# Performance work log

Measured on AMD Instinct MI355X. Metric: run time of the kernel, lower is better.

## Reference

```python
import jax, jax.numpy as jnp
import numpy as np

N_EMBED = 768
NUM_HEADS = 12
HEAD_DIM = N_EMBED // NUM_HEADS
B, L = 4, 2048


def setup_inputs() -> dict:
    key = jax.random.key(0)
    ks = jax.random.split(key, 11)
    s = 0.02
    return {
        "key": jax.random.normal(ks[0], (B, L, N_EMBED), jnp.float32),
        "query": jax.random.normal(ks[1], (B, L, N_EMBED), jnp.float32),
        "value": jax.random.normal(ks[2], (B, L, N_EMBED), jnp.float32),
        "Wk": jax.random.normal(ks[3], (N_EMBED, N_EMBED), jnp.float32) * s,
        "bk": jnp.zeros((N_EMBED,), jnp.float32),
        "Wq": jax.random.normal(ks[4], (N_EMBED, N_EMBED), jnp.float32) * s,
        "bq": jnp.zeros((N_EMBED,), jnp.float32),
        "Wv": jax.random.normal(ks[5], (N_EMBED, N_EMBED), jnp.float32) * s,
        "bv": jnp.zeros((N_EMBED,), jnp.float32),
        "Wfc": jax.random.normal(ks[6], (N_EMBED, N_EMBED), jnp.float32) * s,
        "bfc": jnp.zeros((N_EMBED,), jnp.float32),
    }


def reference(key, query, value, Wk, bk, Wq, bq, Wv, bv, Wfc, bfc):
    # Linear projections (torch Linear: x @ W.T + b)
    k = key @ Wk.T + bk      # [B, Lk, D]
    q = query @ Wq.T + bq    # [B, Lq, D]
    v = value @ Wv.T + bv    # [B, Lv, D]
    Bsz, Lq = q.shape[0], q.shape[1]
    k = k.reshape(Bsz, -1, NUM_HEADS, HEAD_DIM)
    q = q.reshape(Bsz, Lq, NUM_HEADS, HEAD_DIM)
    v = v.reshape(Bsz, -1, NUM_HEADS, HEAD_DIM)
    # Full [B, H, Lq, Lk] score tensor, scaled by sqrt(n_embed) (faithful to source)
    energies = jnp.einsum("nqhd,nkhd->nhqk", q, k)
    attn = jax.nn.softmax(energies / jnp.sqrt(jnp.float32(N_EMBED)), axis=3)
    out = jnp.einsum("nhql,nlhd->nqhd", attn, v).reshape(Bsz, Lq, N_EMBED)
    return out @ Wfc.T + bfc
```

## Files before the change

### kernel.cpp

```cpp
#include <hip/hip_runtime.h>
#include <hip/hip_bf16.h>
#include <math.h>

#define NEMB 768
#define NH   12
#define HD   64
#define BSZ  4
#define SEQ  2048
#define MTOT (BSZ * SEQ)

#define SCALE_LOG2E 0.0520587833f

typedef short bf16x8 __attribute__((ext_vector_type(8)));
typedef short short4v __attribute__((ext_vector_type(4)));
typedef float f32x4 __attribute__((ext_vector_type(4)));
typedef unsigned u32x4 __attribute__((ext_vector_type(4)));

__device__ __forceinline__ short f2bf(float f) {
  __bf16 h = (__bf16)f;
  return __builtin_bit_cast(short, h);
}

__device__ __forceinline__ void g2l16(const short* g, short* l) {
  __builtin_amdgcn_global_load_lds((const __attribute__((address_space(1))) unsigned*)g,
                                   (__attribute__((address_space(3))) unsigned*)l, 16, 0, 0);
}

__device__ __forceinline__ int swz(int x) { return (x ^ (x >> 3)) & 7; }

__global__ __launch_bounds__(256) void cvt_all(
    const float* __restrict__ i0, const float* __restrict__ i1, const float* __restrict__ i2,
    const float* __restrict__ i3, const float* __restrict__ i4, const float* __restrict__ i5,
    const float* __restrict__ i6,
    short* __restrict__ o0, short* __restrict__ o1, short* __restrict__ o2,
    short* __restrict__ o3, short* __restrict__ o4, short* __restrict__ o5,
    short* __restrict__ o6) {
  const int ACT4 = (MTOT * NEMB) / 4;
  const int WGT4 = (NEMB * NEMB) / 4;
  const float* in; short* out; int n4;
  switch (blockIdx.y) {
    case 0: in = i0; out = o0; n4 = ACT4; break;
    case 1: in = i1; out = o1; n4 = ACT4; break;
    case 2: in = i2; out = o2; n4 = ACT4; break;
    case 3: in = i3; out = o3; n4 = WGT4; break;
    case 4: in = i4; out = o4; n4 = WGT4; break;
    case 5: in = i5; out = o5; n4 = WGT4; break;
    default: in = i6; out = o6; n4 = WGT4; break;
  }
  int i = blockIdx.x * 256 + threadIdx.x;
  if (i >= n4) return;
  float4 f = reinterpret_cast<const float4*>(in)[i];
  short4v s; s[0] = f2bf(f.x); s[1] = f2bf(f.y); s[2] = f2bf(f.z); s[3] = f2bf(f.w);
  reinterpret_cast<short4v*>(out)[i] = s;
}

__global__ __launch_bounds__(256) void gemm_qkv(
    const short* __restrict__ A0, const short* __restrict__ A1, const short* __restrict__ A2,
    const short* __restrict__ W0, const short* __restrict__ W1, const short* __restrict__ W2,
    const float* __restrict__ b0, const float* __restrict__ b1, const float* __restrict__ b2,
    short* __restrict__ O0, short* __restrict__ O1, short* __restrict__ O2) {
  __shared__ __align__(16) short As[128 * 32];
  __shared__ __align__(16) short Bs[128 * 32];
  const short* A; const short* W; const float* bias; short* O; float scl;
  switch (blockIdx.z) {
    case 0:  A = A0; W = W0; bias = b0; O = O0; scl = SCALE_LOG2E; break;
    case 1:  A = A1; W = W1; bias = b1; O = O1; scl = 1.f; break;
    default: A = A2; W = W2; bias = b2; O = O2; scl = 1.f; break;
  }
  const int tid = threadIdx.x;
  const int lane = tid & 63, w = tid >> 6;
  const int wr = w >> 1, wc = w & 1;
  const int l15 = lane & 15, l4 = lane >> 4;
  const int m0 = blockIdx.x * 128, n0 = blockIdx.y * 128;

  f32x4 acc[4][4] = {};

  for (int k0 = 0; k0 < NEMB; k0 += 32) {
    __syncthreads();
#pragma unroll
    for (int i = 0; i < 2; ++i) {
      const int idx = tid + i * 256;
      const int row = idx >> 2, u = idx & 3;
      g2l16(A + (size_t)(m0 + row) * NEMB + k0 + u * 8, &As[idx * 8]);
      g2l16(W + (size_t)(n0 + row) * NEMB + k0 + u * 8, &Bs[idx * 8]);
    }
    __syncthreads();

    bf16x8 af[4], bfr[4];
#pragma unroll
    for (int m = 0; m < 4; ++m)
      af[m] = *reinterpret_cast<const bf16x8*>(&As[(wr * 64 + m * 16 + l15) * 32 + l4 * 8]);
#pragma unroll
    for (int n = 0; n < 4; ++n)
      bfr[n] = *reinterpret_cast<const bf16x8*>(&Bs[(wc * 64 + n * 16 + l15) * 32 + l4 * 8]);
#pragma unroll
    for (int m = 0; m < 4; ++m)
#pragma unroll
      for (int n = 0; n < 4; ++n)
        acc[m][n] = __builtin_amdgcn_mfma_f32_16x16x32_bf16(af[m], bfr[n], acc[m][n], 0, 0, 0);
  }

  float bj[4];
#pragma unroll
  for (int n = 0; n < 4; ++n) bj[n] = bias[n0 + wc * 64 + n * 16 + l15];
#pragma unroll
  for (int m = 0; m < 4; ++m)
#pragma unroll
    for (int n = 0; n < 4; ++n) {
      const int col = n0 + wc * 64 + n * 16 + l15;
#pragma unroll
      for (int r = 0; r < 4; ++r) {
        const int row = m0 + wr * 64 + m * 16 + l4 * 4 + r;
        O[(size_t)row * NEMB + col] = f2bf((acc[m][n][r] + bj[n]) * scl);
      }
    }
}

__global__ __launch_bounds__(256) void gemm_fc(
    const short* __restrict__ A, const short* __restrict__ W,
    const float* __restrict__ bias, float* __restrict__ C) {
  __shared__ __align__(16) short As[128 * 32];
  __shared__ __align__(16) short Bs[128 * 32];
  const int tid = threadIdx.x;
  const int lane = tid & 63, w = tid >> 6;
  const int wr = w >> 1, wc = w & 1;
  const int l15 = lane & 15, l4 = lane >> 4;
  const int m0 = blockIdx.x * 128, n0 = blockIdx.y * 128;

  f32x4 acc[4][4] = {};

  for (int k0 = 0; k0 < NEMB; k0 += 32) {
    __syncthreads();
#pragma unroll
    for (int i = 0; i < 2; ++i) {
      const int idx = tid + i * 256;
      const int row = idx >> 2, u = idx & 3;
      g2l16(A + (size_t)(m0 + row) * NEMB + k0 + u * 8, &As[idx * 8]);
      g2l16(W + (size_t)(n0 + row) * NEMB + k0 + u * 8, &Bs[idx * 8]);
    }
    __syncthreads();

    bf16x8 af[4], bfr[4];
#pragma unroll
    for (int m = 0; m < 4; ++m)
      af[m] = *reinterpret_cast<const bf16x8*>(&As[(wr * 64 + m * 16 + l15) * 32 + l4 * 8]);
#pragma unroll
    for (int n = 0; n < 4; ++n)
      bfr[n] = *reinterpret_cast<const bf16x8*>(&Bs[(wc * 64 + n * 16 + l15) * 32 + l4 * 8]);
#pragma unroll
    for (int m = 0; m < 4; ++m)
#pragma unroll
      for (int n = 0; n < 4; ++n)
        acc[m][n] = __builtin_amdgcn_mfma_f32_16x16x32_bf16(af[m], bfr[n], acc[m][n], 0, 0, 0);
  }

  float bj[4];
#pragma unroll
  for (int n = 0; n < 4; ++n) bj[n] = bias[n0 + wc * 64 + n * 16 + l15];
#pragma unroll
  for (int m = 0; m < 4; ++m)
#pragma unroll
    for (int n = 0; n < 4; ++n) {
      const int col = n0 + wc * 64 + n * 16 + l15;
#pragma unroll
      for (int r = 0; r < 4; ++r) {
        const int row = m0 + wr * 64 + m * 16 + l4 * 4 + r;
        C[(size_t)row * NEMB + col] = acc[m][n][r] + bj[n];
      }
    }
}

__global__ __launch_bounds__(256) void attn_mfma(const short* __restrict__ qp, const short* __restrict__ kp,
                                                 const short* __restrict__ vp, short* __restrict__ ao) {
  __shared__ __align__(16) short Ks[64 * 64];
  __shared__ __align__(16) short Vt[64 * 64];
  __shared__ __align__(16) short Ps[4][16 * 72];
  const int tid = threadIdx.x, lane = tid & 63, w = tid >> 6;
  const int l15 = lane & 15, l4 = lane >> 4;
  const int wg = blockIdx.x;
  const int nid = (wg & 7) * 192 + (wg >> 3);
  const int q0 = (nid & 31) * 64;
  const int bh = nid >> 5;
  const int b = bh / NH, h = bh - b * NH;
  const size_t abase = (size_t)b * SEQ * NEMB + h * HD;

  bf16x8 qf[2];
#pragma unroll
  for (int kb = 0; kb < 2; ++kb)
    qf[kb] = *reinterpret_cast<const bf16x8*>(
        &qp[abase + (size_t)(q0 + w * 16 + l15) * NEMB + kb * 32 + l4 * 8]);

  f32x4 o[4] = {};
  float lacc[4] = {0.f, 0.f, 0.f, 0.f};
  const int vd8 = tid & 7, vkv2 = tid >> 3;
  const int vu = vkv2 >> 2, vsub = vkv2 & 3;
  const int pch = l15 >> 3, pcl = l15 & 7;

  for (int kt = 0; kt < SEQ / 64; ++kt) {
    const short* vr = vp + abase + (size_t)(kt * 64 + vkv2 * 2) * NEMB + vd8 * 8;
    bf16x8 v0 = *reinterpret_cast<const bf16x8*>(vr);
    bf16x8 v1 = *reinterpret_cast<const bf16x8*>(vr + NEMB);
    __syncthreads();

#pragma unroll
    for (int i = 0; i < 2; ++i) {
      const int idx = tid + i * 256;
      const int row = idx >> 3, u = idx & 7;
      g2l16(kp + abase + (size_t)(kt * 64 + row) * NEMB + (u ^ swz(row)) * 8, &Ks[idx * 8]);
    }
    {
      u32x4 a0 = __builtin_bit_cast(u32x4, v0);
      u32x4 a1 = __builtin_bit_cast(u32x4, v1);
#pragma unroll
      for (int jj = 0; jj < 4; ++jj) {
        unsigned lo = __builtin_amdgcn_perm(a1[jj], a0[jj], 0x05040100u);
        unsigned hi = __builtin_amdgcn_perm(a1[jj], a0[jj], 0x07060302u);
        const int d0 = vd8 * 8 + jj * 2;
        *reinterpret_cast<unsigned*>(reinterpret_cast<char*>(Vt) + d0 * 128 + (vu ^ swz(d0)) * 16 + vsub * 4) = lo;
        *reinterpret_cast<unsigned*>(reinterpret_cast<char*>(Vt) + (d0 + 1) * 128 + (vu ^ swz(d0 + 1)) * 16 + vsub * 4) = hi;
      }
    }
    __syncthreads();

    f32x4 sf[4];
#pragma unroll
    for (int nf = 0; nf < 4; ++nf) {
      f32x4 a = {0.f, 0.f, 0.f, 0.f};
#pragma unroll
      for (int kb = 0; kb < 2; ++kb) {
        const int row = nf * 16 + l15;
        const int u = kb * 4 + l4;
        bf16x8 kf = *reinterpret_cast<const bf16x8*>(
            reinterpret_cast<char*>(Ks) + row * 128 + (u ^ swz(row)) * 16);
        a = __builtin_amdgcn_mfma_f32_16x16x32_bf16(qf[kb], kf, a, 0, 0, 0);
      }
      sf[nf] = a;
    }

#pragma unroll
    for (int nf = 0; nf < 4; ++nf)
#pragma unroll
      for (int r = 0; r < 4; ++r) {
        const float p = exp2f(sf[nf][r]);
        lacc[r] += p;
        Ps[w][(l4 * 4 + r) * 72 + (((nf * 2 + pch) ^ l4) << 3) + pcl] = f2bf(p);
      }

#pragma unroll
    for (int kb = 0; kb < 2; ++kb) {
      bf16x8 pf = *reinterpret_cast<const bf16x8*>(
          &Ps[w][l15 * 72 + (((kb * 4 + l4) ^ ((l15 >> 2) & 3)) << 3)]);
#pragma unroll
      for (int df = 0; df < 4; ++df) {
        const int d = df * 16 + l15;
        const int u = kb * 4 + l4;
        bf16x8 vf = *reinterpret_cast<const bf16x8*>(
            reinterpret_cast<char*>(Vt) + d * 128 + (u ^ swz(d)) * 16);
        o[df] = __builtin_amdgcn_mfma_f32_16x16x32_bf16(pf, vf, o[df], 0, 0, 0);
      }
    }
  }

#pragma unroll
  for (int r = 0; r < 4; ++r)
#pragma unroll
    for (int off = 1; off < 16; off <<= 1)
      lacc[r] += __shfl_xor(lacc[r], off, 64);

  float inv[4];
#pragma unroll
  for (int r = 0; r < 4; ++r) inv[r] = 1.f / lacc[r];

#pragma unroll
  for (int df = 0; df < 4; ++df)
#pragma unroll
    for (int r = 0; r < 4; ++r) {
      const int row = q0 + w * 16 + l4 * 4 + r;
      ao[abase + (size_t)row * NEMB + df * 16 + l15] = f2bf(o[df][r] * inv[r]);
    }
}

extern "C" void kernel_launch(void* const* d_in, const int* in_sizes, int n_in,
                              void* d_out, int out_size, void* d_ws, size_t ws_size,
                              hipStream_t stream) {
  const float* key   = (const float*)d_in[0];
  const float* query = (const float*)d_in[1];
  const float* value = (const float*)d_in[2];
  const float* Wk    = (const float*)d_in[3];
  const float* bk    = (const float*)d_in[4];
  const float* Wq    = (const float*)d_in[5];
  const float* bq    = (const float*)d_in[6];
  const float* Wv    = (const float*)d_in[7];
  const float* bv    = (const float*)d_in[8];
  const float* Wfc   = (const float*)d_in[9];
  const float* bfc   = (const float*)d_in[10];

  const size_t P = (size_t)MTOT * NEMB;
  const size_t WSZ = (size_t)NEMB * NEMB;
  short* ws  = (short*)d_ws;
  short* qb  = ws;
  short* kb2 = qb + P;
  short* vb2 = kb2 + P;
  short* wq  = vb2 + P;
  short* wk  = wq + WSZ;
  short* wv  = wk + WSZ;
  short* wf  = wv + WSZ;
  short* qpp = wf + WSZ;
  short* kpp = qpp + P;
  short* vpp = kpp + P;
  short* aop = vpp + P;

  cvt_all<<<dim3(P / 4 / 256, 7), 256, 0, stream>>>(
      query, key, value, Wq, Wk, Wv, Wfc, qb, kb2, vb2, wq, wk, wv, wf);

  gemm_qkv<<<dim3(MTOT / 128, NEMB / 128, 3), 256, 0, stream>>>(
      qb, kb2, vb2, wq, wk, wv, bq, bk, bv, qpp, kpp, vpp);

  attn_mfma<<<dim3((SEQ / 64) * BSZ * NH), 256, 0, stream>>>(qpp, kpp, vpp, aop);

  gemm_fc<<<dim3(MTOT / 128, NEMB / 128), 256, 0, stream>>>(aop, wf, bfc, (float*)d_out);
}
```

Measured before the change: 308.4 us.

## Double-buffer GEMM and attention tiles, enlarge attention blocks, shrink fc tile

Both GEMM kernels now double-buffer their LDS tiles, so the next k-slice is prefetched while MFMAs run on the current one, with one barrier per iteration instead of two. The attention kernel moves to 512-thread blocks covering 128 queries. Warps 0-3 stage K via global_load_lds and warps 4-7 load and transpose V into double-buffered LDS, overlapping the loads with compute. gemm_fc uses 128x64 tiles to launch more blocks, at the cost of more LDS per block and possibly lower occupancy.

```diff
diff --git a/kernel.cpp b/kernel.cpp
--- a/kernel.cpp
+++ b/kernel.cpp
@@ -59,8 +59,8 @@
     const short* __restrict__ W0, const short* __restrict__ W1, const short* __restrict__ W2,
     const float* __restrict__ b0, const float* __restrict__ b1, const float* __restrict__ b2,
     short* __restrict__ O0, short* __restrict__ O1, short* __restrict__ O2) {
-  __shared__ __align__(16) short As[128 * 32];
-  __shared__ __align__(16) short Bs[128 * 32];
+  __shared__ __align__(16) short As[2][128 * 32];
+  __shared__ __align__(16) short Bs[2][128 * 32];
   const short* A; const short* W; const float* bias; short* O; float scl;
   switch (blockIdx.z) {
     case 0:  A = A0; W = W0; bias = b0; O = O0; scl = SCALE_LOG2E; break;
@@ -75,29 +75,41 @@
 
   f32x4 acc[4][4] = {};
 
-  for (int k0 = 0; k0 < NEMB; k0 += 32) {
-    __syncthreads();
-#pragma unroll
-    for (int i = 0; i < 2; ++i) {
-      const int idx = tid + i * 256;
-      const int row = idx >> 2, u = idx & 3;
-      g2l16(A + (size_t)(m0 + row) * NEMB + k0 + u * 8, &As[idx * 8]);
-      g2l16(W + (size_t)(n0 + row) * NEMB + k0 + u * 8, &Bs[idx * 8]);
-    }
-    __syncthreads();
-
+#pragma unroll
+  for (int i = 0; i < 2; ++i) {
+    const int idx = tid + i * 256;
+    const int row = idx >> 2, u = idx & 3;
+    g2l16(A + (size_t)(m0 + row) * NEMB + u * 8, &As[0][idx * 8]);
+    g2l16(W + (size_t)(n0 + row) * NEMB + u * 8, &Bs[0][idx * 8]);
+  }
+  __syncthreads();
+
+  const int NT = NEMB / 32;
+  for (int t = 0; t < NT; ++t) {
+    const int cur = t & 1;
+    if (t + 1 < NT) {
+      const int k0 = (t + 1) * 32;
+#pragma unroll
+      for (int i = 0; i < 2; ++i) {
+        const int idx = tid + i * 256;
+        const int row = idx >> 2, u = idx & 3;
+        g2l16(A + (size_t)(m0 + row) * NEMB + k0 + u * 8, &As[cur ^ 1][idx * 8]);
+        g2l16(W + (size_t)(n0 + row) * NEMB + k0 + u * 8, &Bs[cur ^ 1][idx * 8]);
+      }
+    }
     bf16x8 af[4], bfr[4];
 #pragma unroll
     for (int m = 0; m < 4; ++m)
-      af[m] = *reinterpret_cast<const bf16x8*>(&As[(wr * 64 + m * 16 + l15) * 32 + l4 * 8]);
+      af[m] = *reinterpret_cast<const bf16x8*>(&As[cur][(wr * 64 + m * 16 + l15) * 32 + l4 * 8]);
 #pragma unroll
     for (int n = 0; n < 4; ++n)
-      bfr[n] = *reinterpret_cast<const bf16x8*>(&Bs[(wc * 64 + n * 16 + l15) * 32 + l4 * 8]);
+      bfr[n] = *reinterpret_cast<const bf16x8*>(&Bs[cur][(wc * 64 + n * 16 + l15) * 32 + l4 * 8]);
 #pragma unroll
     for (int m = 0; m < 4; ++m)
 #pragma unroll
       for (int n = 0; n < 4; ++n)
         acc[m][n] = __builtin_amdgcn_mfma_f32_16x16x32_bf16(af[m], bfr[n], acc[m][n], 0, 0, 0);
+    __syncthreads();
   }
 
   float bj[4];
@@ -119,68 +131,83 @@
 __global__ __launch_bounds__(256) void gemm_fc(
     const short* __restrict__ A, const short* __restrict__ W,
     const float* __restrict__ bias, float* __restrict__ C) {
-  __shared__ __align__(16) short As[128 * 32];
-  __shared__ __align__(16) short Bs[128 * 32];
+  __shared__ __align__(16) short As[2][128 * 32];
+  __shared__ __align__(16) short Bs[2][64 * 32];
   const int tid = threadIdx.x;
   const int lane = tid & 63, w = tid >> 6;
-  const int wr = w >> 1, wc = w & 1;
   const int l15 = lane & 15, l4 = lane >> 4;
-  const int m0 = blockIdx.x * 128, n0 = blockIdx.y * 128;
-
-  f32x4 acc[4][4] = {};
-
-  for (int k0 = 0; k0 < NEMB; k0 += 32) {
-    __syncthreads();
-#pragma unroll
-    for (int i = 0; i < 2; ++i) {
-      const int idx = tid + i * 256;
-      const int row = idx >> 2, u = idx & 3;
-      g2l16(A + (size_t)(m0 + row) * NEMB + k0 + u * 8, &As[idx * 8]);
-      g2l16(W + (size_t)(n0 + row) * NEMB + k0 + u * 8, &Bs[idx * 8]);
-    }
-    __syncthreads();
-
-    bf16x8 af[4], bfr[4];
-#pragma unroll
-    for (int m = 0; m < 4; ++m)
-      af[m] = *reinterpret_cast<const bf16x8*>(&As[(wr * 64 + m * 16 + l15) * 32 + l4 * 8]);
+  const int m0 = blockIdx.x * 128, n0 = blockIdx.y * 64;
+
+  f32x4 acc[2][4] = {};
+
+#pragma unroll
+  for (int i = 0; i < 2; ++i) {
+    const int idx = tid + i * 256;
+    const int row = idx >> 2, u = idx & 3;
+    g2l16(A + (size_t)(m0 + row) * NEMB + u * 8, &As[0][idx * 8]);
+  }
+  {
+    const int row = tid >> 2, u = tid & 3;
+    g2l16(W + (size_t)(n0 + row) * NEMB + u * 8, &Bs[0][tid * 8]);
+  }
+  __syncthreads();
+
+  const int NT = NEMB / 32;
+  for (int t = 0; t < NT; ++t) {
+    const int cur = t & 1;
+    if (t + 1 < NT) {
+      const int k0 = (t + 1) * 32;
+#pragma unroll
+      for (int i = 0; i < 2; ++i) {
+        const int idx = tid + i * 256;
+        const int row = idx >> 2, u = idx & 3;
+        g2l16(A + (size_t)(m0 + row) * NEMB + k0 + u * 8, &As[cur ^ 1][idx * 8]);
+      }
+      const int row = tid >> 2, u = tid & 3;
+      g2l16(W + (size_t)(n0 + row) * NEMB + k0 + u * 8, &Bs[cur ^ 1][tid * 8]);
+    }
+    bf16x8 af[2], bfr[4];
+#pragma unroll
+    for (int m = 0; m < 2; ++m)
+      af[m] = *reinterpret_cast<const bf16x8*>(&As[cur][(w * 32 + m * 16 + l15) * 32 + l4 * 8]);
 #pragma unroll
     for (int n = 0; n < 4; ++n)
-      bfr[n] = *reinterpret_cast<const bf16x8*>(&Bs[(wc * 64 + n * 16 + l15) * 32 + l4 * 8]);
-#pragma unroll
-    for (int m = 0; m < 4; ++m)
+      bfr[n] = *reinterpret_cast<const bf16x8*>(&Bs[cur][(n * 16 + l15) * 32 + l4 * 8]);
+#pragma unroll
+    for (int m = 0; m < 2; ++m)
 #pragma unroll
       for (int n = 0; n < 4; ++n)
         acc[m][n] = __builtin_amdgcn_mfma_f32_16x16x32_bf16(af[m], bfr[n], acc[m][n], 0, 0, 0);
+    __syncthreads();
   }
 
   float bj[4];
 #pragma unroll
-  for (int n = 0; n < 4; ++n) bj[n] = bias[n0 + wc * 64 + n * 16 + l15];
-#pragma unroll
-  for (int m = 0; m < 4; ++m)
+  for (int n = 0; n < 4; ++n) bj[n] = bias[n0 + n * 16 + l15];
+#pragma unroll
+  for (int m = 0; m < 2; ++m)
 #pragma unroll
     for (int n = 0; n < 4; ++n) {
-      const int col = n0 + wc * 64 + n * 16 + l15;
+      const int col = n0 + n * 16 + l15;
 #pragma unroll
       for (int r = 0; r < 4; ++r) {
-        const int row = m0 + wr * 64 + m * 16 + l4 * 4 + r;
+        const int row = m0 + w * 32 + m * 16 + l4 * 4 + r;
         C[(size_t)row * NEMB + col] = acc[m][n][r] + bj[n];
       }
     }
 }
 
-__global__ __launch_bounds__(256) void attn_mfma(const short* __restrict__ qp, const short* __restrict__ kp,
+__global__ __launch_bounds__(512) void attn_mfma(const short* __restrict__ qp, const short* __restrict__ kp,
                                                  const short* __restrict__ vp, short* __restrict__ ao) {
-  __shared__ __align__(16) short Ks[64 * 64];
-  __shared__ __align__(16) short Vt[64 * 64];
-  __shared__ __align__(16) short Ps[4][16 * 72];
+  __shared__ __align__(16) short Ks[2][64 * 64];
+  __shared__ __align__(16) short Vt[2][64 * 64];
+  __shared__ __align__(16) short Ps[8][16 * 72];
   const int tid = threadIdx.x, lane = tid & 63, w = tid >> 6;
   const int l15 = lane & 15, l4 = lane >> 4;
   const int wg = blockIdx.x;
-  const int nid = (wg & 7) * 192 + (wg >> 3);
-  const int q0 = (nid & 31) * 64;
-  const int bh = nid >> 5;
+  const int nid = (wg & 7) * 96 + (wg >> 3);
+  const int q0 = (nid & 15) * 128;
+  const int bh = nid >> 4;
   const int b = bh / NH, h = bh - b * NH;
   const size_t abase = (size_t)b * SEQ * NEMB + h * HD;
 
@@ -190,25 +217,85 @@
     qf[kb] = *reinterpret_cast<const bf16x8*>(
         &qp[abase + (size_t)(q0 + w * 16 + l15) * NEMB + kb * 32 + l4 * 8]);
 
+  const bool kstager = (w < 4);
+  const int st = tid & 255;
+  const int vkv2 = st >> 3, vd8 = st & 7;
+  const int vu = vkv2 >> 2, vsub = vkv2 & 3;
+  const int pch = l15 >> 3, pcl = l15 & 7;
+
+  if (kstager) {
+#pragma unroll
+    for (int i = 0; i < 2; ++i) {
+      const int idx = st + i * 256;
+      const int row = idx >> 3, u = idx & 7;
+      g2l16(kp + abase + (size_t)row * NEMB + (u ^ swz(row)) * 8, &Ks[0][idx * 8]);
+    }
+  } else {
+    const short* vr = vp + abase + (size_t)(vkv2 * 2) * NEMB + vd8 * 8;
+    bf16x8 v0 = *reinterpret_cast<const bf16x8*>(vr);
+    bf16x8 v1 = *reinterpret_cast<const bf16x8*>(vr + NEMB);
+    u32x4 a0 = __builtin_bit_cast(u32x4, v0);
+    u32x4 a1 = __builtin_bit_cast(u32x4, v1);
+#pragma unroll
+    for (int jj = 0; jj < 4; ++jj) {
+      unsigned lo = __builtin_amdgcn_perm(a1[jj], a0[jj], 0x05040100u);
+      unsigned hi = __builtin_amdgcn_perm(a1[jj], a0[jj], 0x07060302u);
+      const int d0 = vd8 * 8 + jj * 2;
+      *reinterpret_cast<unsigned*>(reinterpret_cast<char*>(Vt[0]) + d0 * 128 + (vu ^ swz(d0)) * 16 + vsub * 4) = lo;
+      *reinterpret_cast<unsigned*>(reinterpret_cast<char*>(Vt[0]) + (d0 + 1) * 128 + (vu ^ swz(d0 + 1)) * 16 + vsub * 4) = hi;
+    }
+  }
+  __syncthreads();
+
   f32x4 o[4] = {};
   float lacc[4] = {0.f, 0.f, 0.f, 0.f};
-  const int vd8 = tid & 7, vkv2 = tid >> 3;
-  const int vu = vkv2 >> 2, vsub = vkv2 & 3;
-  const int pch = l15 >> 3, pcl = l15 & 7;
 
   for (int kt = 0; kt < SEQ / 64; ++kt) {
-    const short* vr = vp + abase + (size_t)(kt * 64 + vkv2 * 2) * NEMB + vd8 * 8;
-    bf16x8 v0 = *reinterpret_cast<const bf16x8*>(vr);
-    bf16x8 v1 = *reinterpret_cast<const bf16x8*>(vr + NEMB);
-    __syncthreads();
-
-#pragma unroll
-    for (int i = 0; i < 2; ++i) {
-      const int idx = tid + i * 256;
-      const int row = idx >> 3, u = idx & 7;
-      g2l16(kp + abase + (size_t)(kt * 64 + row) * NEMB + (u ^ swz(row)) * 8, &Ks[idx * 8]);
-    }
-    {
+    const int cur = kt & 1, nxt = cur ^ 1;
+    const bool more = (kt + 1) < SEQ / 64;
+
+    bf16x8 v0, v1;
+    if (kstager) {
+      if (more) {
+#pragma unroll
+        for (int i = 0; i < 2; ++i) {
+          const int idx = st + i * 256;
+          const int row = idx >> 3, u = idx & 7;
+          g2l16(kp + abase + (size_t)((kt + 1) * 64 + row) * NEMB + (u ^ swz(row)) * 8,
+                &Ks[nxt][idx * 8]);
+        }
+      }
+    } else if (more) {
+      const short* vr = vp + abase + (size_t)((kt + 1) * 64 + vkv2 * 2) * NEMB + vd8 * 8;
+      v0 = *reinterpret_cast<const bf16x8*>(vr);
+      v1 = *reinterpret_cast<const bf16x8*>(vr + NEMB);
+    }
+
+    f32x4 sf[4];
+#pragma unroll
+    for (int nf = 0; nf < 4; ++nf) {
+      f32x4 a = {0.f, 0.f, 0.f, 0.f};
+#pragma unroll
+      for (int kb = 0; kb < 2; ++kb) {
+        const int row = nf * 16 + l15;
+        const int u = kb * 4 + l4;
+        bf16x8 kf = *reinterpret_cast<const bf16x8*>(
+            reinterpret_cast<char*>(Ks[cur]) + row * 128 + (u ^ swz(row)) * 16);
+        a = __builtin_amdgcn_mfma_f32_16x16x32_bf16(qf[kb], kf, a, 0, 0, 0);
+      }
+      sf[nf] = a;
+    }
+
+#pragma unroll
+    for (int nf = 0; nf < 4; ++nf)
+#pragma unroll
+      for (int r = 0; r < 4; ++r) {
+        const float p = exp2f(sf[nf][r]);
+        lacc[r] += p;
+        Ps[w][(l4 * 4 + r) * 72 + (((nf * 2 + pch) ^ l4) << 3) + pcl] = f2bf(p);
+      }
+
+    if (!kstager && more) {
       u32x4 a0 = __builtin_bit_cast(u32x4, v0);
       u32x4 a1 = __builtin_bit_cast(u32x4, v1);
 #pragma unroll
@@ -216,35 +303,10 @@
         unsigned lo = __builtin_amdgcn_perm(a1[jj], a0[jj], 0x05040100u);
         unsigned hi = __builtin_amdgcn_perm(a1[jj], a0[jj], 0x07060302u);
         const int d0 = vd8 * 8 + jj * 2;
-        *reinterpret_cast<unsigned*>(reinterpret_cast<char*>(Vt) + d0 * 128 + (vu ^ swz(d0)) * 16 + vsub * 4) = lo;
-        *reinterpret_cast<unsigned*>(reinterpret_cast<char*>(Vt) + (d0 + 1) * 128 + (vu ^ swz(d0 + 1)) * 16 + vsub * 4) = hi;
-      }
-    }
-    __syncthreads();
-
-    f32x4 sf[4];
-#pragma unroll
-    for (int nf = 0; nf < 4; ++nf) {
-      f32x4 a = {0.f, 0.f, 0.f, 0.f};
-#pragma unroll
-      for (int kb = 0; kb < 2; ++kb) {
-        const int row = nf * 16 + l15;
-        const int u = kb * 4 + l4;
-        bf16x8 kf = *reinterpret_cast<const bf16x8*>(
-            reinterpret_cast<char*>(Ks) + row * 128 + (u ^ swz(row)) * 16);
-        a = __builtin_amdgcn_mfma_f32_16x16x32_bf16(qf[kb], kf, a, 0, 0, 0);
-      }
-      sf[nf] = a;
-    }
-
-#pragma unroll
-    for (int nf = 0; nf < 4; ++nf)
-#pragma unroll
-      for (int r = 0; r < 4; ++r) {
-        const float p = exp2f(sf[nf][r]);
-        lacc[r] += p;
-        Ps[w][(l4 * 4 + r) * 72 + (((nf * 2 + pch) ^ l4) << 3) + pcl] = f2bf(p);
-      }
+        *reinterpret_cast<unsigned*>(reinterpret_cast<char*>(Vt[nxt]) + d0 * 128 + (vu ^ swz(d0)) * 16 + vsub * 4) = lo;
+        *reinterpret_cast<unsigned*>(reinterpret_cast<char*>(Vt[nxt]) + (d0 + 1) * 128 + (vu ^ swz(d0 + 1)) * 16 + vsub * 4) = hi;
+      }
+    }
 
 #pragma unroll
     for (int kb = 0; kb < 2; ++kb) {
@@ -255,10 +317,11 @@
         const int d = df * 16 + l15;
         const int u = kb * 4 + l4;
         bf16x8 vf = *reinterpret_cast<const bf16x8*>(
-            reinterpret_cast<char*>(Vt) + d * 128 + (u ^ swz(d)) * 16);
+            reinterpret_cast<char*>(Vt[cur]) + d * 128 + (u ^ swz(d)) * 16);
         o[df] = __builtin_amdgcn_mfma_f32_16x16x32_bf16(pf, vf, o[df], 0, 0, 0);
       }
     }
+    __syncthreads();
   }
 
 #pragma unroll
@@ -316,7 +379,7 @@
   gemm_qkv<<<dim3(MTOT / 128, NEMB / 128, 3), 256, 0, stream>>>(
       qb, kb2, vb2, wq, wk, wv, bq, bk, bv, qpp, kpp, vpp);
 
-  attn_mfma<<<dim3((SEQ / 64) * BSZ * NH), 256, 0, stream>>>(qpp, kpp, vpp, aop);
-
-  gemm_fc<<<dim3(MTOT / 128, NEMB / 128), 256, 0, stream>>>(aop, wf, bfc, (float*)d_out);
-}
+  attn_mfma<<<dim3(16 * BSZ * NH), 512, 0, stream>>>(qpp, kpp, vpp, aop);
+
+  gemm_fc<<<dim3(MTOT / 128, NEMB / 64), 256, 0, stream>>>(aop, wf, bfc, (float*)d_out);
+}
```

Result: no change. 310.7 us (+0.8%).
